# Kernel tuning notes

Hardware: AMD Instinct MI355X
Metric: run time of the kernel (lower is better)

The kernel has to match this reference:

```python
import jax, jax.numpy as jnp
import numpy as np

N_NODES = 100000
N_EDGES = 1600000
IN_SIZE = 256
OUT_SIZE = 64


def setup_inputs() -> dict:
    key = jax.random.key(0)
    k1, k2, k3 = jax.random.split(key, 3)
    edge_index = jax.random.randint(k1, (2, N_EDGES), 0, N_NODES, dtype=jnp.int32)
    x = jax.random.normal(k2, (N_NODES, IN_SIZE), dtype=jnp.float32)
    W = jax.random.normal(k3, (OUT_SIZE, IN_SIZE), dtype=jnp.float32) * 0.05
    return {"edge_index": edge_index, "x": x, "num_nodes": N_NODES, "W": W}


def reference(edge_index, x, num_nodes, W):
    row, col = edge_index[0], edge_index[1]
    # fill_diag(adj, 1.0): drop any existing diagonal entries (value -> 0),
    # then add exactly one self-loop per node with value 1.0.
    val = jnp.where(row == col, 0.0, 1.0).astype(x.dtype)
    loops = jnp.arange(num_nodes, dtype=row.dtype)
    row_f = jnp.concatenate([row, loops])
    col_f = jnp.concatenate([col, loops])
    val_f = jnp.concatenate([val, jnp.ones((num_nodes,), dtype=x.dtype)])
    # deg = row-sum of adjacency values; D^{-1/2} with inf -> 0
    deg = jax.ops.segment_sum(val_f, row_f, num_segments=num_nodes)
    dinv = jnp.where(deg > 0, deg ** -0.5, 0.0)
    # edge weight: d^{-1/2}[row] * a * d^{-1/2}[col]
    norm = dinv[row_f] * val_f * dinv[col_f]
    # dense projection then SpMM aggregation
    xw = x @ W.T  # [N, out]
    msgs = norm[:, None] * xw[col_f]  # gather over edges [E+N, out]
    out = jax.ops.segment_sum(msgs, row_f, num_segments=num_nodes)
    return out
```

## Files before the change

kernel.cpp:

```cpp
#include <hip/hip_runtime.h>

#define IN_SIZE 256
#define OUT_SIZE 64
#define CAP 10240
#define K1_TILE 4096

typedef __attribute__((ext_vector_type(8))) short short8;
typedef __attribute__((ext_vector_type(4))) float floatx4;

__device__ inline unsigned short f2bf(float f) {
  unsigned u = __builtin_bit_cast(unsigned, f);
  u += 0x7fff + ((u >> 16) & 1);
  return (unsigned short)(u >> 16);
}
__device__ inline float bf2f(unsigned short u) {
  unsigned v = (unsigned)u << 16;
  return __builtin_bit_cast(float, v);
}

__global__ __launch_bounds__(256) void wconv_kernel(const float* __restrict__ W,
                                                    unsigned short* __restrict__ Wb,
                                                    int total) {
  int i = blockIdx.x * 256 + threadIdx.x;
  if (i < total) Wb[i] = f2bf(W[i]);
}

__global__ __launch_bounds__(256) void bucket_coarse_kernel(
    const int* __restrict__ row, const int* __restrict__ col,
    int* __restrict__ coarse_cursor, unsigned* __restrict__ pairs,
    int n_edges, int nbuck) {
  __shared__ int hist[256];
  int tid = threadIdx.x;
  hist[tid] = 0;
  __syncthreads();

  int r[16], c[16];
  int ebase = blockIdx.x * K1_TILE + tid;
#pragma unroll
  for (int i = 0; i < 16; i++) {
    int e = ebase + i * 256;
    bool ok = e < n_edges;
    r[i] = ok ? row[e] : -1;
    c[i] = ok ? col[e] : -1;
    if (ok && r[i] != c[i]) atomicAdd(&hist[r[i] >> 9], 1);
  }
  __syncthreads();

  if (tid < nbuck) {
    int cnt = hist[tid];
    hist[tid] = atomicAdd(&coarse_cursor[tid], cnt);
  }
  __syncthreads();

#pragma unroll
  for (int i = 0; i < 16; i++) {
    if (r[i] >= 0 && r[i] != c[i]) {
      int bin = r[i] >> 9;
      int slot = atomicAdd(&hist[bin], 1);
      if (slot < CAP)
        pairs[(size_t)bin * CAP + slot] =
            ((unsigned)(r[i] & 511) << 17) | (unsigned)c[i];
    }
  }
}

__global__ __launch_bounds__(256) void bucket_fine_kernel(
    const int* __restrict__ coarse_cursor, const unsigned* __restrict__ pairs,
    unsigned* __restrict__ colsp, int* __restrict__ count,
    int* __restrict__ row_start, float* __restrict__ dinv, int n_nodes) {
  __shared__ int hist[512];
  __shared__ int ssum[256];
  int tid = threadIdx.x;
  int b = blockIdx.x;
  size_t base = (size_t)b * CAP;
  int n_b = coarse_cursor[b];
  if (n_b > CAP) n_b = CAP;

  hist[tid] = 0;
  hist[tid + 256] = 0;
  __syncthreads();

  for (int i = tid; i < n_b; i += 256)
    atomicAdd(&hist[pairs[base + i] >> 17], 1);
  __syncthreads();

  int v0 = hist[2 * tid], v1 = hist[2 * tid + 1];
  ssum[tid] = v0 + v1;
  __syncthreads();
  for (int off = 1; off < 256; off <<= 1) {
    int t = (tid >= off) ? ssum[tid - off] : 0;
    __syncthreads();
    ssum[tid] += t;
    __syncthreads();
  }
  int e0 = (tid > 0) ? ssum[tid - 1] : 0;
  int e1 = e0 + v0;

  {
    int r0 = b * 512 + 2 * tid;
    if (r0 < n_nodes) {
      count[r0] = v0;
      row_start[r0] = (int)base + e0;
      dinv[r0] = rsqrtf((float)v0 + 1.0f);
    }
    int r1 = r0 + 1;
    if (r1 < n_nodes) {
      count[r1] = v1;
      row_start[r1] = (int)base + e1;
      dinv[r1] = rsqrtf((float)v1 + 1.0f);
    }
  }
  hist[2 * tid] = e0;
  hist[2 * tid + 1] = e1;
  __syncthreads();

  for (int i = tid; i < n_b; i += 256) {
    unsigned p = pairs[base + i];
    int slot = atomicAdd(&hist[p >> 17], 1);
    colsp[base + slot] = p & 0x1FFFFu;
  }
}

#define WPAD 264
__global__ __launch_bounds__(256) void matmul_kernel(
    const float* __restrict__ x, const unsigned short* __restrict__ Wb,
    const float* __restrict__ dinv, unsigned short* __restrict__ xwd,
    int n_nodes) {
  __shared__ unsigned short w_lds[64][WPAD];

  int tid = threadIdx.x;
  int wave = tid >> 6;
  int lane = tid & 63;
  int quad = lane >> 4;
  int lcol = lane & 15;
  long nbase = (long)blockIdx.x * 64;

  {
    int r = tid >> 2;
    int q = tid & 3;
    const unsigned short* src = Wb + (size_t)r * IN_SIZE + q * 64;
#pragma unroll
    for (int i = 0; i < 8; i++)
      *(short8*)(&w_lds[r][q * 64 + i * 8]) = *(const short8*)(src + i * 8);
  }
  __syncthreads();

  long node = nbase + wave * 16 + lcol;
  long nclamp = (node < (long)n_nodes) ? node : (long)(n_nodes - 1);
  const float* xrow = x + nclamp * IN_SIZE;

  floatx4 acc[4];
#pragma unroll
  for (int t = 0; t < 4; t++) acc[t] = (floatx4){0.f, 0.f, 0.f, 0.f};

#pragma unroll
  for (int kk = 0; kk < 8; kk++) {
    const float* p = xrow + kk * 32 + quad * 8;
    float4 a = *(const float4*)(p);
    float4 bb = *(const float4*)(p + 4);
    short8 bfrag;
    bfrag[0] = (short)f2bf(a.x);  bfrag[1] = (short)f2bf(a.y);
    bfrag[2] = (short)f2bf(a.z);  bfrag[3] = (short)f2bf(a.w);
    bfrag[4] = (short)f2bf(bb.x); bfrag[5] = (short)f2bf(bb.y);
    bfrag[6] = (short)f2bf(bb.z); bfrag[7] = (short)f2bf(bb.w);
#pragma unroll
    for (int t = 0; t < 4; t++) {
      short8 afrag = *(const short8*)(&w_lds[t * 16 + lcol][kk * 32 + quad * 8]);
      acc[t] =
          __builtin_amdgcn_mfma_f32_16x16x32_bf16(afrag, bfrag, acc[t], 0, 0, 0);
    }
  }

  if (node < (long)n_nodes) {
    float dv = dinv[node];
#pragma unroll
    for (int t = 0; t < 4; t++) {
      ushort4 sv;
      sv.x = f2bf(dv * acc[t][0]);
      sv.y = f2bf(dv * acc[t][1]);
      sv.z = f2bf(dv * acc[t][2]);
      sv.w = f2bf(dv * acc[t][3]);
      *(ushort4*)(xwd + node * OUT_SIZE + t * 16 + quad * 4) = sv;
    }
  }
}

__global__ __launch_bounds__(256) void gather_kernel(
    const int* __restrict__ row_start, const int* __restrict__ count,
    const unsigned* __restrict__ colsp, const float* __restrict__ dinv,
    const unsigned short* __restrict__ xwd, float* __restrict__ out,
    int n_nodes) {
  int lane = threadIdx.x & 63;
  int r = blockIdx.x * 4 + (threadIdx.x >> 6);
  if (r >= n_nodes) return;
  int sub = lane & 7;
  int cg = lane >> 3;
  int start = row_start[r];
  int cnt = count[r];

  float acc[8];
#pragma unroll
  for (int i = 0; i < 8; i++) acc[i] = 0.f;

  if (sub == 0) {
    short8 v = *(const short8*)(xwd + (size_t)r * OUT_SIZE + cg * 8);
#pragma unroll
    for (int i = 0; i < 8; i++) acc[i] = bf2f((unsigned short)v[i]);
  }
  for (int j = 0; j < cnt; j += 8) {
    int idx = j + sub;
    bool act = idx < cnt;
    int c = act ? (int)colsp[start + idx] : r;
    short8 v = *(const short8*)(xwd + (size_t)c * OUT_SIZE + cg * 8);
    float m = act ? 1.0f : 0.0f;
#pragma unroll
    for (int i = 0; i < 8; i++) acc[i] += m * bf2f((unsigned short)v[i]);
  }
#pragma unroll
  for (int i = 0; i < 8; i++) {
    acc[i] += __shfl_xor(acc[i], 1);
    acc[i] += __shfl_xor(acc[i], 2);
    acc[i] += __shfl_xor(acc[i], 4);
  }

  if (sub == 0) {
    float dr = dinv[r];
    float4 o0 = make_float4(dr * acc[0], dr * acc[1], dr * acc[2], dr * acc[3]);
    float4 o1 = make_float4(dr * acc[4], dr * acc[5], dr * acc[6], dr * acc[7]);
    float* dst = out + (size_t)r * OUT_SIZE + cg * 8;
    *(float4*)(dst) = o0;
    *(float4*)(dst + 4) = o1;
  }
}

extern "C" void kernel_launch(void* const* d_in, const int* in_sizes, int n_in,
                              void* d_out, int out_size, void* d_ws,
                              size_t ws_size, hipStream_t stream) {
  const int* edge_index = (const int*)d_in[0];
  const float* x = (const float*)d_in[1];
  const float* W = (const float*)d_in[3];

  int n_edges = in_sizes[0] / 2;
  int n_nodes = in_sizes[1] / IN_SIZE;
  const int* row = edge_index;
  const int* col = edge_index + n_edges;
  float* out = (float*)d_out;

  int nbuck = (n_nodes + 511) >> 9;

  char* ws = (char*)d_ws;
  size_t nb = ((size_t)n_nodes * 4 + 15) & ~(size_t)15;
  int* count = (int*)ws;
  int* row_start = (int*)(ws + nb);
  float* dinv = (float*)(ws + 2 * nb);
  int* coarse_cursor = (int*)(ws + 3 * nb);
  size_t bucketsB = (size_t)nbuck * CAP * 4;
  unsigned* pairs = (unsigned*)(ws + 3 * nb + 4096);
  unsigned* colsp = (unsigned*)(ws + 3 * nb + 4096 + bucketsB);
  unsigned short* xwd = (unsigned short*)(ws + 3 * nb + 4096 + 2 * bucketsB);
  unsigned short* Wb =
      (unsigned short*)(ws + 3 * nb + 4096 + 2 * bucketsB +
                        (size_t)n_nodes * OUT_SIZE * 2);

  hipMemsetAsync(coarse_cursor, 0, (size_t)nbuck * 4, stream);

  wconv_kernel<<<(OUT_SIZE * IN_SIZE + 255) / 256, 256, 0, stream>>>(
      W, Wb, OUT_SIZE * IN_SIZE);
  int nb1 = (n_edges + K1_TILE - 1) / K1_TILE;
  bucket_coarse_kernel<<<nb1, 256, 0, stream>>>(row, col, coarse_cursor,
                                                pairs, n_edges, nbuck);
  bucket_fine_kernel<<<nbuck, 256, 0, stream>>>(coarse_cursor, pairs, colsp,
                                                count, row_start, dinv,
                                                n_nodes);
  matmul_kernel<<<(n_nodes + 63) / 64, 256, 0, stream>>>(x, Wb, dinv, xwd,
                                                         n_nodes);
  gather_kernel<<<(n_nodes + 3) / 4, 256, 0, stream>>>(
      row_start, count, colsp, dinv, xwd, out, n_nodes);
}
```

Before: 278.3 us.

## Replace CSR fine sort with per-bucket LDS accumulation of unsorted pairs

```diff
diff --git a/kernel.cpp b/kernel.cpp
--- a/kernel.cpp
+++ b/kernel.cpp
@@ -2,7 +2,10 @@
 
 #define IN_SIZE 256
 #define OUT_SIZE 64
-#define CAP 10240
+#define BSHIFT 7
+#define BROWS 128
+#define BMASK 127
+#define CAP 2560
 #define K1_TILE 4096
 
 typedef __attribute__((ext_vector_type(8))) short short8;
@@ -29,9 +32,10 @@
     const int* __restrict__ row, const int* __restrict__ col,
     int* __restrict__ coarse_cursor, unsigned* __restrict__ pairs,
     int n_edges, int nbuck) {
-  __shared__ int hist[256];
-  int tid = threadIdx.x;
-  hist[tid] = 0;
+  __shared__ int hist[1024];
+  int tid = threadIdx.x;
+#pragma unroll
+  for (int i = 0; i < 4; i++) hist[tid + i * 256] = 0;
   __syncthreads();
 
   int r[16], c[16];
@@ -42,82 +46,45 @@
     bool ok = e < n_edges;
     r[i] = ok ? row[e] : -1;
     c[i] = ok ? col[e] : -1;
-    if (ok && r[i] != c[i]) atomicAdd(&hist[r[i] >> 9], 1);
-  }
-  __syncthreads();
-
-  if (tid < nbuck) {
-    int cnt = hist[tid];
-    hist[tid] = atomicAdd(&coarse_cursor[tid], cnt);
+    if (ok && r[i] != c[i]) atomicAdd(&hist[r[i] >> BSHIFT], 1);
+  }
+  __syncthreads();
+
+  for (int i = tid; i < nbuck; i += 256) {
+    int cnt = hist[i];
+    if (cnt) hist[i] = atomicAdd(&coarse_cursor[i], cnt);
   }
   __syncthreads();
 
 #pragma unroll
   for (int i = 0; i < 16; i++) {
     if (r[i] >= 0 && r[i] != c[i]) {
-      int bin = r[i] >> 9;
+      int bin = r[i] >> BSHIFT;
       int slot = atomicAdd(&hist[bin], 1);
       if (slot < CAP)
         pairs[(size_t)bin * CAP + slot] =
-            ((unsigned)(r[i] & 511) << 17) | (unsigned)c[i];
-    }
-  }
-}
-
-__global__ __launch_bounds__(256) void bucket_fine_kernel(
+            ((unsigned)(r[i] & BMASK) << 17) | (unsigned)c[i];
+    }
+  }
+}
+
+__global__ __launch_bounds__(256) void deg_kernel(
     const int* __restrict__ coarse_cursor, const unsigned* __restrict__ pairs,
-    unsigned* __restrict__ colsp, int* __restrict__ count,
-    int* __restrict__ row_start, float* __restrict__ dinv, int n_nodes) {
-  __shared__ int hist[512];
-  __shared__ int ssum[256];
+    float* __restrict__ dinv, int n_nodes) {
+  __shared__ int hist[BROWS];
   int tid = threadIdx.x;
   int b = blockIdx.x;
+  if (tid < BROWS) hist[tid] = 0;
+  __syncthreads();
   size_t base = (size_t)b * CAP;
   int n_b = coarse_cursor[b];
   if (n_b > CAP) n_b = CAP;
-
-  hist[tid] = 0;
-  hist[tid + 256] = 0;
-  __syncthreads();
-
   for (int i = tid; i < n_b; i += 256)
     atomicAdd(&hist[pairs[base + i] >> 17], 1);
   __syncthreads();
-
-  int v0 = hist[2 * tid], v1 = hist[2 * tid + 1];
-  ssum[tid] = v0 + v1;
-  __syncthreads();
-  for (int off = 1; off < 256; off <<= 1) {
-    int t = (tid >= off) ? ssum[tid - off] : 0;
-    __syncthreads();
-    ssum[tid] += t;
-    __syncthreads();
-  }
-  int e0 = (tid > 0) ? ssum[tid - 1] : 0;
-  int e1 = e0 + v0;
-
-  {
-    int r0 = b * 512 + 2 * tid;
-    if (r0 < n_nodes) {
-      count[r0] = v0;
-      row_start[r0] = (int)base + e0;
-      dinv[r0] = rsqrtf((float)v0 + 1.0f);
-    }
-    int r1 = r0 + 1;
-    if (r1 < n_nodes) {
-      count[r1] = v1;
-      row_start[r1] = (int)base + e1;
-      dinv[r1] = rsqrtf((float)v1 + 1.0f);
-    }
-  }
-  hist[2 * tid] = e0;
-  hist[2 * tid + 1] = e1;
-  __syncthreads();
-
-  for (int i = tid; i < n_b; i += 256) {
-    unsigned p = pairs[base + i];
-    int slot = atomicAdd(&hist[p >> 17], 1);
-    colsp[base + slot] = p & 0x1FFFFu;
+  if (tid < BROWS) {
+    int r = b * BROWS + tid;
+    if (r < n_nodes) dinv[r] = rsqrtf((float)hist[tid] + 1.0f);
   }
 }
 
@@ -185,51 +152,60 @@
   }
 }
 
-__global__ __launch_bounds__(256) void gather_kernel(
-    const int* __restrict__ row_start, const int* __restrict__ count,
-    const unsigned* __restrict__ colsp, const float* __restrict__ dinv,
-    const unsigned short* __restrict__ xwd, float* __restrict__ out,
-    int n_nodes) {
-  int lane = threadIdx.x & 63;
-  int r = blockIdx.x * 4 + (threadIdx.x >> 6);
-  if (r >= n_nodes) return;
-  int sub = lane & 7;
-  int cg = lane >> 3;
-  int start = row_start[r];
-  int cnt = count[r];
-
-  float acc[8];
-#pragma unroll
-  for (int i = 0; i < 8; i++) acc[i] = 0.f;
-
-  if (sub == 0) {
-    short8 v = *(const short8*)(xwd + (size_t)r * OUT_SIZE + cg * 8);
-#pragma unroll
-    for (int i = 0; i < 8; i++) acc[i] = bf2f((unsigned short)v[i]);
-  }
-  for (int j = 0; j < cnt; j += 8) {
-    int idx = j + sub;
-    bool act = idx < cnt;
-    int c = act ? (int)colsp[start + idx] : r;
-    short8 v = *(const short8*)(xwd + (size_t)c * OUT_SIZE + cg * 8);
-    float m = act ? 1.0f : 0.0f;
-#pragma unroll
-    for (int i = 0; i < 8; i++) acc[i] += m * bf2f((unsigned short)v[i]);
-  }
-#pragma unroll
-  for (int i = 0; i < 8; i++) {
-    acc[i] += __shfl_xor(acc[i], 1);
-    acc[i] += __shfl_xor(acc[i], 2);
-    acc[i] += __shfl_xor(acc[i], 4);
-  }
-
-  if (sub == 0) {
-    float dr = dinv[r];
-    float4 o0 = make_float4(dr * acc[0], dr * acc[1], dr * acc[2], dr * acc[3]);
-    float4 o1 = make_float4(dr * acc[4], dr * acc[5], dr * acc[6], dr * acc[7]);
-    float* dst = out + (size_t)r * OUT_SIZE + cg * 8;
-    *(float4*)(dst) = o0;
-    *(float4*)(dst + 4) = o1;
+__global__ __launch_bounds__(256) void aggregate_kernel(
+    const int* __restrict__ coarse_cursor, const unsigned* __restrict__ pairs,
+    const float* __restrict__ dinv, const unsigned short* __restrict__ xwd,
+    float* __restrict__ out, int n_nodes) {
+  __shared__ float acc[BROWS * OUT_SIZE];
+  int tid = threadIdx.x;
+  int wave = tid >> 6;
+  int lane = tid & 63;
+  int b = blockIdx.x;
+
+  {
+    float4* a4 = (float4*)acc;
+    for (int i = tid; i < BROWS * OUT_SIZE / 4; i += 256)
+      a4[i] = make_float4(0.f, 0.f, 0.f, 0.f);
+  }
+  __syncthreads();
+
+  size_t base = (size_t)b * CAP;
+  int n_b = coarse_cursor[b];
+  if (n_b > CAP) n_b = CAP;
+
+  for (int cb = wave * 64; cb < n_b; cb += 256) {
+    int cnt = n_b - cb;
+    if (cnt > 64) cnt = 64;
+    unsigned p = pairs[base + cb + ((lane < cnt) ? lane : 0)];
+    int nfull = cnt & ~7;
+    for (int j0 = 0; j0 < nfull; j0 += 8) {
+      unsigned pj[8];
+      float v[8];
+#pragma unroll
+      for (int u = 0; u < 8; u++) pj[u] = __shfl(p, j0 + u);
+#pragma unroll
+      for (int u = 0; u < 8; u++)
+        v[u] = bf2f(xwd[(size_t)(pj[u] & 0x1FFFFu) * OUT_SIZE + lane]);
+#pragma unroll
+      for (int u = 0; u < 8; u++)
+        atomicAdd(&acc[(pj[u] >> 17) * OUT_SIZE + lane], v[u]);
+    }
+    for (int j = nfull; j < cnt; j++) {
+      unsigned pj = __shfl(p, j);
+      float v = bf2f(xwd[(size_t)(pj & 0x1FFFFu) * OUT_SIZE + lane]);
+      atomicAdd(&acc[(pj >> 17) * OUT_SIZE + lane], v);
+    }
+  }
+  __syncthreads();
+
+  int rbase = b * BROWS;
+  for (int i = wave; i < BROWS; i += 4) {
+    int r = rbase + i;
+    if (r < n_nodes) {
+      float dr = dinv[r];
+      float self = bf2f(xwd[(size_t)r * OUT_SIZE + lane]);
+      out[(size_t)r * OUT_SIZE + lane] = dr * (acc[i * OUT_SIZE + lane] + self);
+    }
   }
 }
 
@@ -246,21 +222,17 @@
   const int* col = edge_index + n_edges;
   float* out = (float*)d_out;
 
-  int nbuck = (n_nodes + 511) >> 9;
+  int nbuck = (n_nodes + BROWS - 1) >> BSHIFT;
 
   char* ws = (char*)d_ws;
   size_t nb = ((size_t)n_nodes * 4 + 15) & ~(size_t)15;
-  int* count = (int*)ws;
-  int* row_start = (int*)(ws + nb);
-  float* dinv = (float*)(ws + 2 * nb);
-  int* coarse_cursor = (int*)(ws + 3 * nb);
+  float* dinv = (float*)ws;
+  int* coarse_cursor = (int*)(ws + nb);
+  unsigned* pairs = (unsigned*)(ws + nb + 4096);
   size_t bucketsB = (size_t)nbuck * CAP * 4;
-  unsigned* pairs = (unsigned*)(ws + 3 * nb + 4096);
-  unsigned* colsp = (unsigned*)(ws + 3 * nb + 4096 + bucketsB);
-  unsigned short* xwd = (unsigned short*)(ws + 3 * nb + 4096 + 2 * bucketsB);
-  unsigned short* Wb =
-      (unsigned short*)(ws + 3 * nb + 4096 + 2 * bucketsB +
-                        (size_t)n_nodes * OUT_SIZE * 2);
+  unsigned short* xwd = (unsigned short*)(ws + nb + 4096 + bucketsB);
+  unsigned short* Wb = (unsigned short*)(ws + nb + 4096 + bucketsB +
+                                         (size_t)n_nodes * OUT_SIZE * 2);
 
   hipMemsetAsync(coarse_cursor, 0, (size_t)nbuck * 4, stream);
 
@@ -269,11 +241,9 @@
   int nb1 = (n_edges + K1_TILE - 1) / K1_TILE;
   bucket_coarse_kernel<<<nb1, 256, 0, stream>>>(row, col, coarse_cursor,
                                                 pairs, n_edges, nbuck);
-  bucket_fine_kernel<<<nbuck, 256, 0, stream>>>(coarse_cursor, pairs, colsp,
-                                                count, row_start, dinv,
-                                                n_nodes);
+  deg_kernel<<<nbuck, 256, 0, stream>>>(coarse_cursor, pairs, dinv, n_nodes);
   matmul_kernel<<<(n_nodes + 63) / 64, 256, 0, stream>>>(x, Wb, dinv, xwd,
                                                          n_nodes);
-  gather_kernel<<<(n_nodes + 3) / 4, 256, 0, stream>>>(
-      row_start, count, colsp, dinv, xwd, out, n_nodes);
-}
+  aggregate_kernel<<<nbuck, 256, 0, stream>>>(coarse_cursor, pairs, dinv, xwd,
+                                              out, n_nodes);
+}
```

Result: slower. 920.5 us (+230.8%).

## Use finer 128-row buckets and process four rows per wave in gather

Applied to the files above, without the earlier changes.

```diff
diff --git a/kernel.cpp b/kernel.cpp
--- a/kernel.cpp
+++ b/kernel.cpp
@@ -2,7 +2,10 @@
 
 #define IN_SIZE 256
 #define OUT_SIZE 64
-#define CAP 10240
+#define BSHIFT 7
+#define BROWS 128
+#define BMASK 127
+#define CAP 2560
 #define K1_TILE 4096
 
 typedef __attribute__((ext_vector_type(8))) short short8;
@@ -29,9 +32,10 @@
     const int* __restrict__ row, const int* __restrict__ col,
     int* __restrict__ coarse_cursor, unsigned* __restrict__ pairs,
     int n_edges, int nbuck) {
-  __shared__ int hist[256];
+  __shared__ int hist[1024];
   int tid = threadIdx.x;
-  hist[tid] = 0;
+#pragma unroll
+  for (int i = 0; i < 4; i++) hist[tid + i * 256] = 0;
   __syncthreads();
 
   int r[16], c[16];
@@ -42,24 +46,24 @@
     bool ok = e < n_edges;
     r[i] = ok ? row[e] : -1;
     c[i] = ok ? col[e] : -1;
-    if (ok && r[i] != c[i]) atomicAdd(&hist[r[i] >> 9], 1);
-  }
-  __syncthreads();
-
-  if (tid < nbuck) {
-    int cnt = hist[tid];
-    hist[tid] = atomicAdd(&coarse_cursor[tid], cnt);
+    if (ok && r[i] != c[i]) atomicAdd(&hist[r[i] >> BSHIFT], 1);
+  }
+  __syncthreads();
+
+  for (int i = tid; i < nbuck; i += 256) {
+    int cnt = hist[i];
+    if (cnt) hist[i] = atomicAdd(&coarse_cursor[i], cnt);
   }
   __syncthreads();
 
 #pragma unroll
   for (int i = 0; i < 16; i++) {
     if (r[i] >= 0 && r[i] != c[i]) {
-      int bin = r[i] >> 9;
+      int bin = r[i] >> BSHIFT;
       int slot = atomicAdd(&hist[bin], 1);
       if (slot < CAP)
         pairs[(size_t)bin * CAP + slot] =
-            ((unsigned)(r[i] & 511) << 17) | (unsigned)c[i];
+            ((unsigned)(r[i] & BMASK) << 17) | (unsigned)c[i];
     }
   }
 }
@@ -68,50 +72,41 @@
     const int* __restrict__ coarse_cursor, const unsigned* __restrict__ pairs,
     unsigned* __restrict__ colsp, int* __restrict__ count,
     int* __restrict__ row_start, float* __restrict__ dinv, int n_nodes) {
-  __shared__ int hist[512];
-  __shared__ int ssum[256];
+  __shared__ int hist[BROWS];
+  __shared__ int scn[BROWS];
   int tid = threadIdx.x;
   int b = blockIdx.x;
   size_t base = (size_t)b * CAP;
   int n_b = coarse_cursor[b];
   if (n_b > CAP) n_b = CAP;
 
-  hist[tid] = 0;
-  hist[tid + 256] = 0;
+  if (tid < BROWS) hist[tid] = 0;
   __syncthreads();
 
   for (int i = tid; i < n_b; i += 256)
     atomicAdd(&hist[pairs[base + i] >> 17], 1);
   __syncthreads();
 
-  int v0 = hist[2 * tid], v1 = hist[2 * tid + 1];
-  ssum[tid] = v0 + v1;
-  __syncthreads();
-  for (int off = 1; off < 256; off <<= 1) {
-    int t = (tid >= off) ? ssum[tid - off] : 0;
+  if (tid < BROWS) scn[tid] = hist[tid];
+  __syncthreads();
+  for (int off = 1; off < BROWS; off <<= 1) {
+    int t = (tid >= off && tid < BROWS) ? scn[tid - off] : 0;
     __syncthreads();
-    ssum[tid] += t;
+    if (tid < BROWS) scn[tid] += t;
     __syncthreads();
   }
-  int e0 = (tid > 0) ? ssum[tid - 1] : 0;
-  int e1 = e0 + v0;
-
-  {
-    int r0 = b * 512 + 2 * tid;
-    if (r0 < n_nodes) {
-      count[r0] = v0;
-      row_start[r0] = (int)base + e0;
-      dinv[r0] = rsqrtf((float)v0 + 1.0f);
-    }
-    int r1 = r0 + 1;
-    if (r1 < n_nodes) {
-      count[r1] = v1;
-      row_start[r1] = (int)base + e1;
-      dinv[r1] = rsqrtf((float)v1 + 1.0f);
-    }
-  }
-  hist[2 * tid] = e0;
-  hist[2 * tid + 1] = e1;
+
+  if (tid < BROWS) {
+    int e = (tid > 0) ? scn[tid - 1] : 0;
+    int r = b * BROWS + tid;
+    if (r < n_nodes) {
+      int deg = hist[tid];
+      count[r] = deg;
+      row_start[r] = (int)base + e;
+      dinv[r] = rsqrtf((float)deg + 1.0f);
+    }
+    hist[tid] = e;
+  }
   __syncthreads();
 
   for (int i = tid; i < n_b; i += 256) {
@@ -191,45 +186,86 @@
     const unsigned short* __restrict__ xwd, float* __restrict__ out,
     int n_nodes) {
   int lane = threadIdx.x & 63;
-  int r = blockIdx.x * 4 + (threadIdx.x >> 6);
-  if (r >= n_nodes) return;
+  int wave = threadIdx.x >> 6;
   int sub = lane & 7;
   int cg = lane >> 3;
-  int start = row_start[r];
-  int cnt = count[r];
-
-  float acc[8];
-#pragma unroll
-  for (int i = 0; i < 8; i++) acc[i] = 0.f;
+  int rb = (blockIdx.x * 4 + wave) * 4;
+  if (rb >= n_nodes) return;
+
+  int start[4], cnt[4];
+  int maxc = 0;
+#pragma unroll
+  for (int i = 0; i < 4; i++) {
+    int r = rb + i;
+    bool ok = r < n_nodes;
+    start[i] = ok ? row_start[r] : 0;
+    cnt[i] = ok ? count[r] : 0;
+    maxc = max(maxc, cnt[i]);
+  }
+
+  float acc[4][8];
+#pragma unroll
+  for (int i = 0; i < 4; i++)
+#pragma unroll
+    for (int k = 0; k < 8; k++) acc[i][k] = 0.f;
 
   if (sub == 0) {
-    short8 v = *(const short8*)(xwd + (size_t)r * OUT_SIZE + cg * 8);
-#pragma unroll
-    for (int i = 0; i < 8; i++) acc[i] = bf2f((unsigned short)v[i]);
-  }
-  for (int j = 0; j < cnt; j += 8) {
+#pragma unroll
+    for (int i = 0; i < 4; i++) {
+      int r = rb + i;
+      if (r < n_nodes) {
+        short8 v = *(const short8*)(xwd + (size_t)r * OUT_SIZE + cg * 8);
+#pragma unroll
+        for (int k = 0; k < 8; k++) acc[i][k] = bf2f((unsigned short)v[k]);
+      }
+    }
+  }
+
+  for (int j = 0; j < maxc; j += 8) {
+    int c[4];
+    float m[4];
     int idx = j + sub;
-    bool act = idx < cnt;
-    int c = act ? (int)colsp[start + idx] : r;
-    short8 v = *(const short8*)(xwd + (size_t)c * OUT_SIZE + cg * 8);
-    float m = act ? 1.0f : 0.0f;
-#pragma unroll
-    for (int i = 0; i < 8; i++) acc[i] += m * bf2f((unsigned short)v[i]);
-  }
-#pragma unroll
-  for (int i = 0; i < 8; i++) {
-    acc[i] += __shfl_xor(acc[i], 1);
-    acc[i] += __shfl_xor(acc[i], 2);
-    acc[i] += __shfl_xor(acc[i], 4);
-  }
+#pragma unroll
+    for (int i = 0; i < 4; i++) {
+      bool act = idx < cnt[i];
+      c[i] = act ? (int)colsp[start[i] + idx] : rb;
+      m[i] = act ? 1.0f : 0.0f;
+    }
+    short8 v[4];
+#pragma unroll
+    for (int i = 0; i < 4; i++)
+      v[i] = *(const short8*)(xwd + (size_t)c[i] * OUT_SIZE + cg * 8);
+#pragma unroll
+    for (int i = 0; i < 4; i++)
+#pragma unroll
+      for (int k = 0; k < 8; k++)
+        acc[i][k] += m[i] * bf2f((unsigned short)v[i][k]);
+  }
+
+#pragma unroll
+  for (int i = 0; i < 4; i++)
+#pragma unroll
+    for (int k = 0; k < 8; k++) {
+      acc[i][k] += __shfl_xor(acc[i][k], 1);
+      acc[i][k] += __shfl_xor(acc[i][k], 2);
+      acc[i][k] += __shfl_xor(acc[i][k], 4);
+    }
 
   if (sub == 0) {
-    float dr = dinv[r];
-    float4 o0 = make_float4(dr * acc[0], dr * acc[1], dr * acc[2], dr * acc[3]);
-    float4 o1 = make_float4(dr * acc[4], dr * acc[5], dr * acc[6], dr * acc[7]);
-    float* dst = out + (size_t)r * OUT_SIZE + cg * 8;
-    *(float4*)(dst) = o0;
-    *(float4*)(dst + 4) = o1;
+#pragma unroll
+    for (int i = 0; i < 4; i++) {
+      int r = rb + i;
+      if (r < n_nodes) {
+        float dr = dinv[r];
+        float* dst = out + (size_t)r * OUT_SIZE + cg * 8;
+        *(float4*)(dst) =
+            make_float4(dr * acc[i][0], dr * acc[i][1], dr * acc[i][2],
+                        dr * acc[i][3]);
+        *(float4*)(dst + 4) =
+            make_float4(dr * acc[i][4], dr * acc[i][5], dr * acc[i][6],
+                        dr * acc[i][7]);
+      }
+    }
   }
 }
 
@@ -246,7 +282,7 @@
   const int* col = edge_index + n_edges;
   float* out = (float*)d_out;
 
-  int nbuck = (n_nodes + 511) >> 9;
+  int nbuck = (n_nodes + BROWS - 1) >> BSHIFT;
 
   char* ws = (char*)d_ws;
   size_t nb = ((size_t)n_nodes * 4 + 15) & ~(size_t)15;
@@ -257,7 +293,8 @@
   size_t bucketsB = (size_t)nbuck * CAP * 4;
   unsigned* pairs = (unsigned*)(ws + 3 * nb + 4096);
   unsigned* colsp = (unsigned*)(ws + 3 * nb + 4096 + bucketsB);
-  unsigned short* xwd = (unsigned short*)(ws + 3 * nb + 4096 + 2 * bucketsB);
+  unsigned short* xwd =
+      (unsigned short*)(ws + 3 * nb + 4096 + 2 * bucketsB);
   unsigned short* Wb =
       (unsigned short*)(ws + 3 * nb + 4096 + 2 * bucketsB +
                         (size_t)n_nodes * OUT_SIZE * 2);
@@ -274,6 +311,6 @@
                                                 n_nodes);
   matmul_kernel<<<(n_nodes + 63) / 64, 256, 0, stream>>>(x, Wb, dinv, xwd,
                                                          n_nodes);
-  gather_kernel<<<(n_nodes + 3) / 4, 256, 0, stream>>>(
+  gather_kernel<<<(n_nodes + 15) / 16, 256, 0, stream>>>(
       row_start, count, colsp, dinv, xwd, out, n_nodes);
 }
```

Result: no change. 273.3 us (-1.8%).
